# Kernel optimization log

Hardware: AMD Instinct MI355X
Metric: run time of the kernel (lower is better)

## Reference

```python
import jax, jax.numpy as jnp
import numpy as np

N = 256      # n_nodes (complete graph -> E = N*N edges)
HID = 128    # hid_dim
L = 4        # num_layers
NCAT = 64    # number of edge-orbit categories
CIN, COUT = 2, 3
B = 8
E = N * N


def _ln(x, g, b, eps=1e-5):
    m = x.mean(-1, keepdims=True)
    v = ((x - m) ** 2).mean(-1, keepdims=True)
    return (x - m) * jax.lax.rsqrt(v + eps) * g + b


def _mlp(x, W1, b1, g1, bt1, W2, b2, g2, bt2):
    # Linear -> LayerNorm -> ReLU -> Linear -> LayerNorm
    h = jax.nn.relu(_ln(x @ W1 + b1, g1, bt1))
    return _ln(h @ W2 + b2, g2, bt2)


def setup_inputs() -> dict:
    key = jax.random.key(0)
    ks = jax.random.split(key, 10)
    s = 0.05
    ii = jnp.arange(N, dtype=jnp.int32)
    edge_src = jnp.repeat(ii, N)   # i of (i,j), matches [(i,j) for i for j]
    edge_dst = jnp.tile(ii, N)     # j of (i,j)
    edge_cat = jax.random.randint(ks[0], (E,), 0, NCAT, dtype=jnp.int32)
    return dict(
        x=jax.random.normal(ks[1], (B, N, CIN), jnp.float32),
        emb=jax.random.normal(ks[2], (NCAT, HID), jnp.float32),
        in_W1=jax.random.normal(ks[3], (CIN, HID), jnp.float32) * s,
        in_b1=jnp.zeros(HID), in_g1=jnp.ones(HID), in_bt1=jnp.zeros(HID),
        in_W2=jax.random.normal(ks[4], (HID, HID), jnp.float32) * s,
        in_b2=jnp.zeros(HID), in_g2=jnp.ones(HID), in_bt2=jnp.zeros(HID),
        conv_W1=jax.random.normal(ks[5], (L, HID, HID), jnp.float32) * s,
        conv_b1=jnp.zeros((L, HID)), conv_g1=jnp.ones((L, HID)), conv_bt1=jnp.zeros((L, HID)),
        conv_W2=jax.random.normal(ks[6], (L, HID, HID), jnp.float32) * s,
        conv_b2=jnp.zeros((L, HID)), conv_g2=jnp.ones((L, HID)), conv_bt2=jnp.zeros((L, HID)),
        conv_eps=jnp.zeros(L),
        ln_g=jnp.ones((L, HID)), ln_b=jnp.zeros((L, HID)),
        out_W=jax.random.normal(ks[7], (HID, COUT), jnp.float32) * s,
        out_b=jnp.zeros(COUT),
        edge_src=edge_src, edge_dst=edge_dst, edge_cat=edge_cat,
    )


def reference(x, emb, in_W1, in_b1, in_g1, in_bt1, in_W2, in_b2, in_g2, in_bt2,
              conv_W1, conv_b1, conv_g1, conv_bt1, conv_W2, conv_b2, conv_g2, conv_bt2,
              conv_eps, ln_g, ln_b, out_W, out_b, edge_src, edge_dst, edge_cat):
    # EdgeEmbedder: per-category max-norm clip (all norms = 1.0 in the dense path)
    e = emb[edge_cat]                                  # [E, HID]
    cn = jnp.linalg.norm(e, axis=1, keepdims=True)
    cn = jnp.where(cn == 0, 1e-8, cn)
    e = e * jnp.minimum(1.0, 1.0 / cn)

    def item(xi):                                      # xi: [N, CIN]
        h = _mlp(xi, in_W1, in_b1, in_g1, in_bt1, in_W2, in_b2, in_g2, in_bt2)
        for l in range(L):
            # GINEConv: msg = relu(x_j + e_ij), aggregate (sum) at destination
            msg = jax.nn.relu(h[edge_src] + e)          # [E, HID]
            agg = jax.ops.segment_sum(msg, edge_dst, num_segments=N)
            h2 = _mlp((1.0 + conv_eps[l]) * h + agg,
                      conv_W1[l], conv_b1[l], conv_g1[l], conv_bt1[l],
                      conv_W2[l], conv_b2[l], conv_g2[l], conv_bt2[l])
            h = jax.nn.relu(_ln(h2, ln_g[l], ln_b[l])) + h
        return h @ out_W + out_b                        # [N, COUT]

    return jax.vmap(item)(x)                            # [B, N, COUT]
```

## Files before the change

### kernel.cpp

```cpp
#include <hip/hip_runtime.h>

#define HID 128
#define NN  256
#define BB  8
#define NCATS 64

__device__ inline void ln_stats(float a, float c, float& mean, float& rs) {
    float s = a + c;
    float q = a * a + c * c;
    #pragma unroll
    for (int m = 32; m; m >>= 1) {
        s += __shfl_xor(s, m);
        q += __shfl_xor(q, m);
    }
    mean = s * (1.0f / 128.0f);
    float var = q * (1.0f / 128.0f) - mean * mean;
    rs = rsqrtf(var + 1e-5f);
}

__global__ __launch_bounds__(512) void k_setup(
    const float* __restrict__ x, const float* __restrict__ emb,
    const float* __restrict__ inW1, const float* __restrict__ inb1,
    const float* __restrict__ ing1, const float* __restrict__ inbt1,
    const float* __restrict__ inW2, const float* __restrict__ inb2,
    const float* __restrict__ ing2, const float* __restrict__ inbt2,
    const int* __restrict__ ecat,
    float* __restrict__ ne, uint2* __restrict__ catp, float* __restrict__ h0)
{
    __shared__ __align__(16) float sV[8][128];
    __shared__ __align__(16) float sH1[8][128];
    __shared__ __align__(16) float sA[4][8][128];

    const int blk = blockIdx.x;
    const int t = threadIdx.x;
    const int w = t >> 6, lane = t & 63;

    if (blk < 256) {
        const int row0 = blk * 8;
        for (int item = t; item < 1024; item += 512) {
            int r = item >> 7, dd = item & 127;
            int row = row0 + r;
            float x0 = x[row * 2 + 0], x1 = x[row * 2 + 1];
            sV[r][dd] = fmaf(x0, inW1[dd], fmaf(x1, inW1[128 + dd], inb1[dd]));
        }
        __syncthreads();
        {
            float a = sV[w][lane], c = sV[w][lane + 64];
            float mean, rs; ln_stats(a, c, mean, rs);
            sH1[w][lane]      = fmaxf((a - mean) * rs * ing1[lane]      + inbt1[lane],      0.f);
            sH1[w][lane + 64] = fmaxf((c - mean) * rs * ing1[lane + 64] + inbt1[lane + 64], 0.f);
        }
        __syncthreads();
        {
            int dd = t & 127, ks = t >> 7;
            float acc[8] = {0.f, 0.f, 0.f, 0.f, 0.f, 0.f, 0.f, 0.f};
            for (int k = ks * 32; k < ks * 32 + 32; ++k) {
                float wv = inW2[k * 128 + dd];
                #pragma unroll
                for (int r = 0; r < 8; ++r) acc[r] = fmaf(sH1[r][k], wv, acc[r]);
            }
            #pragma unroll
            for (int r = 0; r < 8; ++r) sA[ks][r][dd] = acc[r];
        }
        __syncthreads();
        for (int item = t; item < 1024; item += 512) {
            int r = item >> 7, dd = item & 127;
            sV[r][dd] = inb2[dd] + sA[0][r][dd] + sA[1][r][dd] + sA[2][r][dd] + sA[3][r][dd];
        }
        __syncthreads();
        {
            float a = sV[w][lane], c = sV[w][lane + 64];
            float mean, rs; ln_stats(a, c, mean, rs);
            int row = row0 + w;
            h0[row * HID + lane]      = (a - mean) * rs * ing2[lane]      + inbt2[lane];
            h0[row * HID + lane + 64] = (c - mean) * rs * ing2[lane + 64] + inbt2[lane + 64];
        }
    } else if (blk < 264) {
        int r = (blk - 256) * 8 + w;
        float a = emb[r * 128 + lane], c = emb[r * 128 + lane + 64];
        float q = a * a + c * c;
        #pragma unroll
        for (int m = 32; m; m >>= 1) q += __shfl_xor(q, m);
        float cn = sqrtf(q);
        if (cn == 0.f) cn = 1e-8f;
        float sc = fminf(1.0f, 1.0f / cn);
        ne[r * 128 + lane]      = a * sc;
        ne[r * 128 + lane + 64] = c * sc;
    } else {
        int jb = blk - 264;
        if (t < 256) {
            int i = t;
            const int* p = ecat + i * NN + jb * 8;
            int4 c0 = *(const int4*)p;
            int4 c1 = *(const int4*)(p + 4);
            unsigned lo = (unsigned)c0.x | ((unsigned)c0.y << 8) |
                          ((unsigned)c0.z << 16) | ((unsigned)c0.w << 24);
            unsigned hi = (unsigned)c1.x | ((unsigned)c1.y << 8) |
                          ((unsigned)c1.z << 16) | ((unsigned)c1.w << 24);
            catp[jb * 256 + i] = make_uint2(lo, hi);
        }
    }
}

__global__ __launch_bounds__(512) void k_layer(
    const float* __restrict__ h_old, float* __restrict__ h_new,
    const float* __restrict__ ne, const uint2* __restrict__ catp,
    const float* __restrict__ W1, const float* __restrict__ b1,
    const float* __restrict__ g1, const float* __restrict__ bt1,
    const float* __restrict__ W2, const float* __restrict__ b2,
    const float* __restrict__ g2, const float* __restrict__ bt2,
    const float* __restrict__ epsp,
    const float* __restrict__ lng, const float* __restrict__ lnb,
    const float* __restrict__ outW, const float* __restrict__ outb,
    float* __restrict__ dout, int isLast)
{
    __shared__ __align__(16) float sNe[NCATS * HID];
    __shared__ __align__(16) float sAcc[16 * 8 * 128];
    __shared__ __align__(16) uint2 sCat[256];
    __shared__ __align__(16) float sU[8][128];
    __shared__ __align__(16) float sH1[8][128];
    __shared__ __align__(16) float sV[8][128];

    const int t = threadIdx.x;
    const int b = blockIdx.x >> 5;
    const int jb = blockIdx.x & 31;
    const int w = t >> 6, lane = t & 63;
    const float* hb = h_old + (size_t)b * NN * HID;

    for (int idx = t; idx < NCATS * HID / 4; idx += 512)
        ((float4*)sNe)[idx] = ((const float4*)ne)[idx];
    if (t < 256) sCat[t] = catp[jb * 256 + t];
    __syncthreads();

    const int dg = t & 31;
    const int ig = t >> 5;
    float4 acc[8];
    #pragma unroll
    for (int k = 0; k < 8; ++k) acc[k] = make_float4(0.f, 0.f, 0.f, 0.f);

    for (int n = 0; n < 16; ++n) {
        int i = ig * 16 + n;
        float4 hv = *(const float4*)(hb + i * HID + dg * 4);
        uint2 c8 = sCat[i];
        #pragma unroll
        for (int k = 0; k < 8; ++k) {
            unsigned c = ((k < 4 ? (c8.x >> (8 * k)) : (c8.y >> (8 * (k - 4)))) & 255u);
            float4 nv = *(const float4*)&sNe[c * HID + dg * 4];
            acc[k].x += fmaxf(hv.x + nv.x, 0.f);
            acc[k].y += fmaxf(hv.y + nv.y, 0.f);
            acc[k].z += fmaxf(hv.z + nv.z, 0.f);
            acc[k].w += fmaxf(hv.w + nv.w, 0.f);
        }
    }
    #pragma unroll
    for (int k = 0; k < 8; ++k)
        *(float4*)&sAcc[(ig * 8 + k) * 128 + dg * 4] = acc[k];
    __syncthreads();

    const float eps1 = 1.0f + epsp[0];
    for (int item = t; item < 1024; item += 512) {
        int r = item >> 7, dd = item & 127;
        float s = 0.f;
        #pragma unroll
        for (int igx = 0; igx < 16; ++igx) s += sAcc[(igx * 8 + r) * 128 + dd];
        sU[r][dd] = eps1 * hb[(jb * 8 + r) * HID + dd] + s;
    }
    __syncthreads();

    {
        int dd = t & 127, ks = t >> 7;
        float a8[8] = {0.f, 0.f, 0.f, 0.f, 0.f, 0.f, 0.f, 0.f};
        for (int k = ks * 32; k < ks * 32 + 32; ++k) {
            float wv = W1[k * 128 + dd];
            #pragma unroll
            for (int r = 0; r < 8; ++r) a8[r] = fmaf(sU[r][k], wv, a8[r]);
        }
        #pragma unroll
        for (int r = 0; r < 8; ++r) sAcc[(ks * 8 + r) * 128 + dd] = a8[r];
    }
    __syncthreads();
    for (int item = t; item < 1024; item += 512) {
        int r = item >> 7, dd = item & 127;
        sV[r][dd] = b1[dd] + sAcc[r * 128 + dd] + sAcc[(8 + r) * 128 + dd] +
                    sAcc[(16 + r) * 128 + dd] + sAcc[(24 + r) * 128 + dd];
    }
    __syncthreads();

    {
        float a = sV[w][lane], c = sV[w][lane + 64];
        float mean, rs; ln_stats(a, c, mean, rs);
        sH1[w][lane]      = fmaxf((a - mean) * rs * g1[lane]      + bt1[lane],      0.f);
        sH1[w][lane + 64] = fmaxf((c - mean) * rs * g1[lane + 64] + bt1[lane + 64], 0.f);
    }
    __syncthreads();

    {
        int dd = t & 127, ks = t >> 7;
        float a8[8] = {0.f, 0.f, 0.f, 0.f, 0.f, 0.f, 0.f, 0.f};
        for (int k = ks * 32; k < ks * 32 + 32; ++k) {
            float wv = W2[k * 128 + dd];
            #pragma unroll
            for (int r = 0; r < 8; ++r) a8[r] = fmaf(sH1[r][k], wv, a8[r]);
        }
        #pragma unroll
        for (int r = 0; r < 8; ++r) sAcc[(ks * 8 + r) * 128 + dd] = a8[r];
    }
    __syncthreads();
    for (int item = t; item < 1024; item += 512) {
        int r = item >> 7, dd = item & 127;
        sV[r][dd] = b2[dd] + sAcc[r * 128 + dd] + sAcc[(8 + r) * 128 + dd] +
                    sAcc[(16 + r) * 128 + dd] + sAcc[(24 + r) * 128 + dd];
    }
    __syncthreads();

    {
        float a = sV[w][lane], c = sV[w][lane + 64];
        float mean, rs; ln_stats(a, c, mean, rs);
        float y1 = (a - mean) * rs * g2[lane]      + bt2[lane];
        float y2 = (c - mean) * rs * g2[lane + 64] + bt2[lane + 64];

        float mean3, rs3; ln_stats(y1, y2, mean3, rs3);
        int row = jb * 8 + w;
        int grow = b * NN + row;
        float ho1 = hb[row * HID + lane], ho2 = hb[row * HID + lane + 64];
        float z1 = fmaxf((y1 - mean3) * rs3 * lng[lane]      + lnb[lane],      0.f) + ho1;
        float z2 = fmaxf((y2 - mean3) * rs3 * lng[lane + 64] + lnb[lane + 64], 0.f) + ho2;

        if (!isLast) {
            h_new[(size_t)grow * HID + lane]      = z1;
            h_new[(size_t)grow * HID + lane + 64] = z2;
        } else {
            #pragma unroll
            for (int cc = 0; cc < 3; ++cc) {
                float p = z1 * outW[lane * 3 + cc] + z2 * outW[(lane + 64) * 3 + cc];
                #pragma unroll
                for (int m = 32; m; m >>= 1) p += __shfl_xor(p, m);
                if (lane == 0) dout[grow * 3 + cc] = p + outb[cc];
            }
        }
    }
}

extern "C" void kernel_launch(void* const* d_in, const int* in_sizes, int n_in,
                              void* d_out, int out_size, void* d_ws, size_t ws_size,
                              hipStream_t stream) {
    const float* x     = (const float*)d_in[0];
    const float* emb   = (const float*)d_in[1];
    const float* inW1  = (const float*)d_in[2];
    const float* inb1  = (const float*)d_in[3];
    const float* ing1  = (const float*)d_in[4];
    const float* inbt1 = (const float*)d_in[5];
    const float* inW2  = (const float*)d_in[6];
    const float* inb2  = (const float*)d_in[7];
    const float* ing2  = (const float*)d_in[8];
    const float* inbt2 = (const float*)d_in[9];
    const float* cW1   = (const float*)d_in[10];
    const float* cb1   = (const float*)d_in[11];
    const float* cg1   = (const float*)d_in[12];
    const float* cbt1  = (const float*)d_in[13];
    const float* cW2   = (const float*)d_in[14];
    const float* cb2   = (const float*)d_in[15];
    const float* cg2   = (const float*)d_in[16];
    const float* cbt2  = (const float*)d_in[17];
    const float* ceps  = (const float*)d_in[18];
    const float* lng   = (const float*)d_in[19];
    const float* lnb   = (const float*)d_in[20];
    const float* outW  = (const float*)d_in[21];
    const float* outb  = (const float*)d_in[22];
    const int*   ecat  = (const int*)d_in[25];

    float* ws   = (float*)d_ws;
    float* ne   = ws;
    uint2* catp = (uint2*)(ws + 8192);
    float* hA   = ws + 8192 + 16384;
    float* hB   = hA + BB * NN * HID;
    float* out  = (float*)d_out;

    k_setup<<<296, 512, 0, stream>>>(x, emb, inW1, inb1, ing1, inbt1,
                                     inW2, inb2, ing2, inbt2, ecat, ne, catp, hA);

    for (int l = 0; l < 4; ++l) {
        const float* ho = (l & 1) ? hB : hA;
        float*       hn = (l & 1) ? hA : hB;
        k_layer<<<256, 512, 0, stream>>>(
            ho, hn, ne, catp,
            cW1 + l * HID * HID, cb1 + l * HID, cg1 + l * HID, cbt1 + l * HID,
            cW2 + l * HID * HID, cb2 + l * HID, cg2 + l * HID, cbt2 + l * HID,
            ceps + l, lng + l * HID, lnb + l * HID,
            outW, outb, out, (l == 3) ? 1 : 0);
    }
}
```

Before: 74.44 us.

## Fuse setup and all layers into one cooperative kernel with bf16 operands

Merges the setup kernel and the four layer kernels into one persistent cooperative kernel that uses grid.sync between layers. It also stores the normalized edge embeddings and the matmul activations as bf16 in shared memory, and pads the embedding layout. The gather partial sums are now reduced with a cross-half shuffle, which halves the shared-memory partial buffer. This removes launch overhead and the global round-trip for the embedding and category tables, at the cost of bf16 precision loss and a dependence on cooperative-launch support, with a multi-launch fallback.

```diff
diff --git a/kernel.cpp b/kernel.cpp
--- a/kernel.cpp
+++ b/kernel.cpp
@@ -1,9 +1,22 @@
 #include <hip/hip_runtime.h>
+#include <hip/hip_cooperative_groups.h>
+
+namespace cg = cooperative_groups;
 
 #define HID 128
 #define NN  256
 #define BB  8
 #define NCATS 64
+
+__device__ inline unsigned pack_bf16(float lo, float hi) {
+    unsigned ul = __float_as_uint(lo);
+    unsigned uh = __float_as_uint(hi);
+    ul = (ul + 0x7fffu + ((ul >> 16) & 1u)) >> 16;
+    uh = (uh + 0x7fffu + ((uh >> 16) & 1u)) & 0xffff0000u;
+    return ul | uh;
+}
+__device__ inline float bf_lo(unsigned v) { return __uint_as_float(v << 16); }
+__device__ inline float bf_hi(unsigned v) { return __uint_as_float(v & 0xffff0000u); }
 
 __device__ inline void ln_stats(float a, float c, float& mean, float& rs) {
     float s = a + c;
@@ -18,275 +31,333 @@
     rs = rsqrtf(var + 1e-5f);
 }
 
-__global__ __launch_bounds__(512) void k_setup(
-    const float* __restrict__ x, const float* __restrict__ emb,
-    const float* __restrict__ inW1, const float* __restrict__ inb1,
-    const float* __restrict__ ing1, const float* __restrict__ inbt1,
-    const float* __restrict__ inW2, const float* __restrict__ inb2,
-    const float* __restrict__ ing2, const float* __restrict__ inbt2,
-    const int* __restrict__ ecat,
-    float* __restrict__ ne, uint2* __restrict__ catp, float* __restrict__ h0)
+struct KArgs {
+    const float* x; const float* emb;
+    const float* inW1; const float* inb1; const float* ing1; const float* inbt1;
+    const float* inW2; const float* inb2; const float* ing2; const float* inbt2;
+    const float* cW1; const float* cb1; const float* cg1; const float* cbt1;
+    const float* cW2; const float* cb2; const float* cg2; const float* cbt2;
+    const float* ceps; const float* lng; const float* lnb;
+    const float* outW; const float* outb;
+    const int* ecat;
+    float* hA; float* hB; float* dout;
+};
+
+__global__ __launch_bounds__(512, 2) void k_fused(KArgs a, int lbeg, int lend, int dosync)
 {
-    __shared__ __align__(16) float sV[8][128];
-    __shared__ __align__(16) float sH1[8][128];
-    __shared__ __align__(16) float sA[4][8][128];
-
-    const int blk = blockIdx.x;
-    const int t = threadIdx.x;
-    const int w = t >> 6, lane = t & 63;
-
-    if (blk < 256) {
-        const int row0 = blk * 8;
-        for (int item = t; item < 1024; item += 512) {
-            int r = item >> 7, dd = item & 127;
-            int row = row0 + r;
-            float x0 = x[row * 2 + 0], x1 = x[row * 2 + 1];
-            sV[r][dd] = fmaf(x0, inW1[dd], fmaf(x1, inW1[128 + dd], inb1[dd]));
-        }
-        __syncthreads();
-        {
-            float a = sV[w][lane], c = sV[w][lane + 64];
-            float mean, rs; ln_stats(a, c, mean, rs);
-            sH1[w][lane]      = fmaxf((a - mean) * rs * ing1[lane]      + inbt1[lane],      0.f);
-            sH1[w][lane + 64] = fmaxf((c - mean) * rs * ing1[lane + 64] + inbt1[lane + 64], 0.f);
-        }
-        __syncthreads();
-        {
-            int dd = t & 127, ks = t >> 7;
-            float acc[8] = {0.f, 0.f, 0.f, 0.f, 0.f, 0.f, 0.f, 0.f};
-            for (int k = ks * 32; k < ks * 32 + 32; ++k) {
-                float wv = inW2[k * 128 + dd];
-                #pragma unroll
-                for (int r = 0; r < 8; ++r) acc[r] = fmaf(sH1[r][k], wv, acc[r]);
-            }
-            #pragma unroll
-            for (int r = 0; r < 8; ++r) sA[ks][r][dd] = acc[r];
-        }
-        __syncthreads();
-        for (int item = t; item < 1024; item += 512) {
-            int r = item >> 7, dd = item & 127;
-            sV[r][dd] = inb2[dd] + sA[0][r][dd] + sA[1][r][dd] + sA[2][r][dd] + sA[3][r][dd];
-        }
-        __syncthreads();
-        {
-            float a = sV[w][lane], c = sV[w][lane + 64];
-            float mean, rs; ln_stats(a, c, mean, rs);
-            int row = row0 + w;
-            h0[row * HID + lane]      = (a - mean) * rs * ing2[lane]      + inbt2[lane];
-            h0[row * HID + lane + 64] = (c - mean) * rs * ing2[lane + 64] + inbt2[lane + 64];
-        }
-    } else if (blk < 264) {
-        int r = (blk - 256) * 8 + w;
-        float a = emb[r * 128 + lane], c = emb[r * 128 + lane + 64];
-        float q = a * a + c * c;
+    __shared__ __align__(16) uint4    sNe4[NCATS * 17];
+    __shared__ __align__(16) float    sPart[8 * 8 * 128];
+    __shared__ __align__(16) uint2    sCat[256];
+    __shared__ __align__(16) uint4    sUT[128];
+    __shared__ __align__(16) float    sH1[8][128];
+    __shared__ __align__(16) uint4    sH1T[128];
+    __shared__ __align__(16) float    sV[8][128];
+
+    cg::grid_group grid = cg::this_grid();
+
+    const int t  = threadIdx.x;
+    const int b  = blockIdx.x >> 5;
+    const int jg = blockIdx.x & 31;
+    const int w  = t >> 6, lane = t & 63;
+    const uint2* sNe2 = (const uint2*)sNe4;
+
+    #pragma unroll 1
+    for (int rr = 0; rr < 8; ++rr) {
+        int r = w * 8 + rr;
+        float2 em = *(const float2*)(a.emb + r * 128 + 2 * lane);
+        float q = em.x * em.x + em.y * em.y;
         #pragma unroll
         for (int m = 32; m; m >>= 1) q += __shfl_xor(q, m);
         float cn = sqrtf(q);
         if (cn == 0.f) cn = 1e-8f;
         float sc = fminf(1.0f, 1.0f / cn);
-        ne[r * 128 + lane]      = a * sc;
-        ne[r * 128 + lane + 64] = c * sc;
-    } else {
-        int jb = blk - 264;
-        if (t < 256) {
-            int i = t;
-            const int* p = ecat + i * NN + jb * 8;
-            int4 c0 = *(const int4*)p;
-            int4 c1 = *(const int4*)(p + 4);
-            unsigned lo = (unsigned)c0.x | ((unsigned)c0.y << 8) |
-                          ((unsigned)c0.z << 16) | ((unsigned)c0.w << 24);
-            unsigned hi = (unsigned)c1.x | ((unsigned)c1.y << 8) |
-                          ((unsigned)c1.z << 16) | ((unsigned)c1.w << 24);
-            catp[jb * 256 + i] = make_uint2(lo, hi);
-        }
-    }
-}
-
-__global__ __launch_bounds__(512) void k_layer(
-    const float* __restrict__ h_old, float* __restrict__ h_new,
-    const float* __restrict__ ne, const uint2* __restrict__ catp,
-    const float* __restrict__ W1, const float* __restrict__ b1,
-    const float* __restrict__ g1, const float* __restrict__ bt1,
-    const float* __restrict__ W2, const float* __restrict__ b2,
-    const float* __restrict__ g2, const float* __restrict__ bt2,
-    const float* __restrict__ epsp,
-    const float* __restrict__ lng, const float* __restrict__ lnb,
-    const float* __restrict__ outW, const float* __restrict__ outb,
-    float* __restrict__ dout, int isLast)
-{
-    __shared__ __align__(16) float sNe[NCATS * HID];
-    __shared__ __align__(16) float sAcc[16 * 8 * 128];
-    __shared__ __align__(16) uint2 sCat[256];
-    __shared__ __align__(16) float sU[8][128];
-    __shared__ __align__(16) float sH1[8][128];
-    __shared__ __align__(16) float sV[8][128];
-
-    const int t = threadIdx.x;
-    const int b = blockIdx.x >> 5;
-    const int jb = blockIdx.x & 31;
-    const int w = t >> 6, lane = t & 63;
-    const float* hb = h_old + (size_t)b * NN * HID;
-
-    for (int idx = t; idx < NCATS * HID / 4; idx += 512)
-        ((float4*)sNe)[idx] = ((const float4*)ne)[idx];
-    if (t < 256) sCat[t] = catp[jb * 256 + t];
+        ((unsigned*)sNe4)[r * 68 + lane] = pack_bf16(em.x * sc, em.y * sc);
+    }
+    if (t < 256) {
+        const int* p = a.ecat + t * NN + jg * 8;
+        int4 c0 = *(const int4*)p;
+        int4 c1 = *(const int4*)(p + 4);
+        unsigned lo = (unsigned)c0.x | ((unsigned)c0.y << 8) |
+                      ((unsigned)c0.z << 16) | ((unsigned)c0.w << 24);
+        unsigned hi = (unsigned)c1.x | ((unsigned)c1.y << 8) |
+                      ((unsigned)c1.z << 16) | ((unsigned)c1.w << 24);
+        sCat[t] = make_uint2(lo, hi);
+    }
     __syncthreads();
 
-    const int dg = t & 31;
-    const int ig = t >> 5;
-    float4 acc[8];
-    #pragma unroll
-    for (int k = 0; k < 8; ++k) acc[k] = make_float4(0.f, 0.f, 0.f, 0.f);
-
-    for (int n = 0; n < 16; ++n) {
-        int i = ig * 16 + n;
-        float4 hv = *(const float4*)(hb + i * HID + dg * 4);
-        uint2 c8 = sCat[i];
+    if (lbeg < 0) {
+        for (int item = t; item < 1024; item += 512) {
+            int r = item >> 7, d = item & 127;
+            int row = b * NN + jg * 8 + r;
+            float x0 = a.x[row * 2 + 0], x1 = a.x[row * 2 + 1];
+            sV[r][d] = fmaf(x0, a.inW1[d], fmaf(x1, a.inW1[128 + d], a.inb1[d]));
+        }
+        __syncthreads();
+        {
+            float aa = sV[w][lane], cc = sV[w][lane + 64];
+            float mean, rs; ln_stats(aa, cc, mean, rs);
+            sH1[w][lane]      = fmaxf((aa - mean) * rs * a.ing1[lane]      + a.inbt1[lane],      0.f);
+            sH1[w][lane + 64] = fmaxf((cc - mean) * rs * a.ing1[lane + 64] + a.inbt1[lane + 64], 0.f);
+        }
+        __syncthreads();
+        {
+            int dim = t & 127, q = t >> 7;
+            ((unsigned*)sH1T)[dim * 4 + q] = pack_bf16(sH1[2 * q][dim], sH1[2 * q + 1][dim]);
+        }
+        __syncthreads();
+        {
+            const int dd = t & 127, ks = t >> 7;
+            float a8[8] = {0.f,0.f,0.f,0.f,0.f,0.f,0.f,0.f};
+            #pragma unroll 8
+            for (int k = 0; k < 32; ++k) {
+                int kk = ks * 32 + k;
+                uint4 ax = sH1T[kk];
+                float wv = a.inW2[kk * 128 + dd];
+                a8[0] = fmaf(bf_lo(ax.x), wv, a8[0]);
+                a8[1] = fmaf(bf_hi(ax.x), wv, a8[1]);
+                a8[2] = fmaf(bf_lo(ax.y), wv, a8[2]);
+                a8[3] = fmaf(bf_hi(ax.y), wv, a8[3]);
+                a8[4] = fmaf(bf_lo(ax.z), wv, a8[4]);
+                a8[5] = fmaf(bf_hi(ax.z), wv, a8[5]);
+                a8[6] = fmaf(bf_lo(ax.w), wv, a8[6]);
+                a8[7] = fmaf(bf_hi(ax.w), wv, a8[7]);
+            }
+            #pragma unroll
+            for (int r = 0; r < 8; ++r) sPart[(ks * 8 + r) * 128 + dd] = a8[r];
+        }
+        __syncthreads();
+        for (int item = t; item < 1024; item += 512) {
+            int r = item >> 7, d = item & 127;
+            sV[r][d] = a.inb2[d] + sPart[r * 128 + d] + sPart[(8 + r) * 128 + d] +
+                       sPart[(16 + r) * 128 + d] + sPart[(24 + r) * 128 + d];
+        }
+        __syncthreads();
+        {
+            float aa = sV[w][lane], cc = sV[w][lane + 64];
+            float mean, rs; ln_stats(aa, cc, mean, rs);
+            int grow = b * NN + jg * 8 + w;
+            a.hA[grow * HID + lane]      = (aa - mean) * rs * a.ing2[lane]      + a.inbt2[lane];
+            a.hA[grow * HID + lane + 64] = (cc - mean) * rs * a.ing2[lane + 64] + a.inbt2[lane + 64];
+        }
+        if (dosync) grid.sync();
+    }
+
+    #pragma unroll 1
+    for (int l = (lbeg < 0 ? 0 : lbeg); l < lend; ++l) {
+        const float* h_old = (l & 1) ? a.hB : a.hA;
+        float*       h_new = (l & 1) ? a.hA : a.hB;
+        const float* W1  = a.cW1 + l * HID * HID;
+        const float* W2  = a.cW2 + l * HID * HID;
+        const float* b1  = a.cb1 + l * HID;
+        const float* b2  = a.cb2 + l * HID;
+        const float* g1  = a.cg1 + l * HID;
+        const float* bt1 = a.cbt1 + l * HID;
+        const float* g2  = a.cg2 + l * HID;
+        const float* bt2 = a.cbt2 + l * HID;
+        const float* lg  = a.lng + l * HID;
+        const float* lb  = a.lnb + l * HID;
+        const float* hb  = h_old + (size_t)b * NN * HID;
+        const int isLast = (l == 3);
+
+        const int dg = t & 31;
+        const int ig = t >> 5;
+        float acc[8][4];
         #pragma unroll
-        for (int k = 0; k < 8; ++k) {
-            unsigned c = ((k < 4 ? (c8.x >> (8 * k)) : (c8.y >> (8 * (k - 4)))) & 255u);
-            float4 nv = *(const float4*)&sNe[c * HID + dg * 4];
-            acc[k].x += fmaxf(hv.x + nv.x, 0.f);
-            acc[k].y += fmaxf(hv.y + nv.y, 0.f);
-            acc[k].z += fmaxf(hv.z + nv.z, 0.f);
-            acc[k].w += fmaxf(hv.w + nv.w, 0.f);
-        }
-    }
-    #pragma unroll
-    for (int k = 0; k < 8; ++k)
-        *(float4*)&sAcc[(ig * 8 + k) * 128 + dg * 4] = acc[k];
-    __syncthreads();
-
-    const float eps1 = 1.0f + epsp[0];
-    for (int item = t; item < 1024; item += 512) {
-        int r = item >> 7, dd = item & 127;
-        float s = 0.f;
+        for (int k = 0; k < 8; ++k)
+            #pragma unroll
+            for (int d = 0; d < 4; ++d) acc[k][d] = 0.f;
+
+        #pragma unroll 4
+        for (int n = 0; n < 16; ++n) {
+            int i = ig * 16 + n;
+            float4 hv = *(const float4*)(hb + i * HID + dg * 4);
+            uint2 c8 = sCat[i];
+            #pragma unroll
+            for (int k = 0; k < 8; ++k) {
+                unsigned c = ((k < 4 ? (c8.x >> (8 * k)) : (c8.y >> (8 * (k - 4)))) & 255u);
+                uint2 nv = sNe2[c * 34 + dg];
+                acc[k][0] += fmaxf(hv.x + bf_lo(nv.x), 0.f);
+                acc[k][1] += fmaxf(hv.y + bf_hi(nv.x), 0.f);
+                acc[k][2] += fmaxf(hv.z + bf_lo(nv.y), 0.f);
+                acc[k][3] += fmaxf(hv.w + bf_hi(nv.y), 0.f);
+            }
+        }
         #pragma unroll
-        for (int igx = 0; igx < 16; ++igx) s += sAcc[(igx * 8 + r) * 128 + dd];
-        sU[r][dd] = eps1 * hb[(jb * 8 + r) * HID + dd] + s;
-    }
-    __syncthreads();
-
-    {
-        int dd = t & 127, ks = t >> 7;
-        float a8[8] = {0.f, 0.f, 0.f, 0.f, 0.f, 0.f, 0.f, 0.f};
-        for (int k = ks * 32; k < ks * 32 + 32; ++k) {
-            float wv = W1[k * 128 + dd];
-            #pragma unroll
-            for (int r = 0; r < 8; ++r) a8[r] = fmaf(sU[r][k], wv, a8[r]);
-        }
-        #pragma unroll
-        for (int r = 0; r < 8; ++r) sAcc[(ks * 8 + r) * 128 + dd] = a8[r];
-    }
-    __syncthreads();
-    for (int item = t; item < 1024; item += 512) {
-        int r = item >> 7, dd = item & 127;
-        sV[r][dd] = b1[dd] + sAcc[r * 128 + dd] + sAcc[(8 + r) * 128 + dd] +
-                    sAcc[(16 + r) * 128 + dd] + sAcc[(24 + r) * 128 + dd];
-    }
-    __syncthreads();
-
-    {
-        float a = sV[w][lane], c = sV[w][lane + 64];
-        float mean, rs; ln_stats(a, c, mean, rs);
-        sH1[w][lane]      = fmaxf((a - mean) * rs * g1[lane]      + bt1[lane],      0.f);
-        sH1[w][lane + 64] = fmaxf((c - mean) * rs * g1[lane + 64] + bt1[lane + 64], 0.f);
-    }
-    __syncthreads();
-
-    {
-        int dd = t & 127, ks = t >> 7;
-        float a8[8] = {0.f, 0.f, 0.f, 0.f, 0.f, 0.f, 0.f, 0.f};
-        for (int k = ks * 32; k < ks * 32 + 32; ++k) {
-            float wv = W2[k * 128 + dd];
-            #pragma unroll
-            for (int r = 0; r < 8; ++r) a8[r] = fmaf(sH1[r][k], wv, a8[r]);
-        }
-        #pragma unroll
-        for (int r = 0; r < 8; ++r) sAcc[(ks * 8 + r) * 128 + dd] = a8[r];
-    }
-    __syncthreads();
-    for (int item = t; item < 1024; item += 512) {
-        int r = item >> 7, dd = item & 127;
-        sV[r][dd] = b2[dd] + sAcc[r * 128 + dd] + sAcc[(8 + r) * 128 + dd] +
-                    sAcc[(16 + r) * 128 + dd] + sAcc[(24 + r) * 128 + dd];
-    }
-    __syncthreads();
-
-    {
-        float a = sV[w][lane], c = sV[w][lane + 64];
-        float mean, rs; ln_stats(a, c, mean, rs);
-        float y1 = (a - mean) * rs * g2[lane]      + bt2[lane];
-        float y2 = (c - mean) * rs * g2[lane + 64] + bt2[lane + 64];
-
-        float mean3, rs3; ln_stats(y1, y2, mean3, rs3);
-        int row = jb * 8 + w;
-        int grow = b * NN + row;
-        float ho1 = hb[row * HID + lane], ho2 = hb[row * HID + lane + 64];
-        float z1 = fmaxf((y1 - mean3) * rs3 * lng[lane]      + lnb[lane],      0.f) + ho1;
-        float z2 = fmaxf((y2 - mean3) * rs3 * lng[lane + 64] + lnb[lane + 64], 0.f) + ho2;
-
-        if (!isLast) {
-            h_new[(size_t)grow * HID + lane]      = z1;
-            h_new[(size_t)grow * HID + lane + 64] = z2;
-        } else {
-            #pragma unroll
-            for (int cc = 0; cc < 3; ++cc) {
-                float p = z1 * outW[lane * 3 + cc] + z2 * outW[(lane + 64) * 3 + cc];
+        for (int k = 0; k < 8; ++k)
+            #pragma unroll
+            for (int d = 0; d < 4; ++d)
+                acc[k][d] += __shfl_xor(acc[k][d], 32);
+        {
+            int kb = ((t >> 5) & 1) * 4;
+            #pragma unroll
+            for (int k2 = 0; k2 < 4; ++k2)
+                *(float4*)&sPart[(w * 8 + kb + k2) * 128 + dg * 4] =
+                    make_float4(acc[kb + k2][0], acc[kb + k2][1],
+                                acc[kb + k2][2], acc[kb + k2][3]);
+        }
+        __syncthreads();
+
+        {
+            int dim = t & 127, q = t >> 7;
+            const float eps1 = 1.0f + a.ceps[l];
+            int r0 = 2 * q, r1 = 2 * q + 1;
+            float u0 = eps1 * hb[(jg * 8 + r0) * HID + dim];
+            float u1 = eps1 * hb[(jg * 8 + r1) * HID + dim];
+            #pragma unroll
+            for (int pg = 0; pg < 8; ++pg) {
+                u0 += sPart[(pg * 8 + r0) * 128 + dim];
+                u1 += sPart[(pg * 8 + r1) * 128 + dim];
+            }
+            ((unsigned*)sUT)[dim * 4 + q] = pack_bf16(u0, u1);
+        }
+        __syncthreads();
+
+        {
+            const int dd = t & 127, ks = t >> 7;
+            float a8[8] = {0.f,0.f,0.f,0.f,0.f,0.f,0.f,0.f};
+            #pragma unroll 8
+            for (int k = 0; k < 32; ++k) {
+                int kk = ks * 32 + k;
+                uint4 ax = sUT[kk];
+                float wv = W1[kk * 128 + dd];
+                a8[0] = fmaf(bf_lo(ax.x), wv, a8[0]);
+                a8[1] = fmaf(bf_hi(ax.x), wv, a8[1]);
+                a8[2] = fmaf(bf_lo(ax.y), wv, a8[2]);
+                a8[3] = fmaf(bf_hi(ax.y), wv, a8[3]);
+                a8[4] = fmaf(bf_lo(ax.z), wv, a8[4]);
+                a8[5] = fmaf(bf_hi(ax.z), wv, a8[5]);
+                a8[6] = fmaf(bf_lo(ax.w), wv, a8[6]);
+                a8[7] = fmaf(bf_hi(ax.w), wv, a8[7]);
+            }
+            #pragma unroll
+            for (int r = 0; r < 8; ++r) sPart[(ks * 8 + r) * 128 + dd] = a8[r];
+        }
+        __syncthreads();
+        for (int item = t; item < 1024; item += 512) {
+            int r = item >> 7, d = item & 127;
+            sV[r][d] = b1[d] + sPart[r * 128 + d] + sPart[(8 + r) * 128 + d] +
+                       sPart[(16 + r) * 128 + d] + sPart[(24 + r) * 128 + d];
+        }
+        __syncthreads();
+
+        {
+            float aa = sV[w][lane], cc = sV[w][lane + 64];
+            float mean, rs; ln_stats(aa, cc, mean, rs);
+            sH1[w][lane]      = fmaxf((aa - mean) * rs * g1[lane]      + bt1[lane],      0.f);
+            sH1[w][lane + 64] = fmaxf((cc - mean) * rs * g1[lane + 64] + bt1[lane + 64], 0.f);
+        }
+        __syncthreads();
+        {
+            int dim = t & 127, q = t >> 7;
+            ((unsigned*)sH1T)[dim * 4 + q] = pack_bf16(sH1[2 * q][dim], sH1[2 * q + 1][dim]);
+        }
+        __syncthreads();
+
+        {
+            const int dd = t & 127, ks = t >> 7;
+            float a8[8] = {0.f,0.f,0.f,0.f,0.f,0.f,0.f,0.f};
+            #pragma unroll 8
+            for (int k = 0; k < 32; ++k) {
+                int kk = ks * 32 + k;
+                uint4 ax = sH1T[kk];
+                float wv = W2[kk * 128 + dd];
+                a8[0] = fmaf(bf_lo(ax.x), wv, a8[0]);
+                a8[1] = fmaf(bf_hi(ax.x), wv, a8[1]);
+                a8[2] = fmaf(bf_lo(ax.y), wv, a8[2]);
+                a8[3] = fmaf(bf_hi(ax.y), wv, a8[3]);
+                a8[4] = fmaf(bf_lo(ax.z), wv, a8[4]);
+                a8[5] = fmaf(bf_hi(ax.z), wv, a8[5]);
+                a8[6] = fmaf(bf_lo(ax.w), wv, a8[6]);
+                a8[7] = fmaf(bf_hi(ax.w), wv, a8[7]);
+            }
+            #pragma unroll
+            for (int r = 0; r < 8; ++r) sPart[(ks * 8 + r) * 128 + dd] = a8[r];
+        }
+        __syncthreads();
+        for (int item = t; item < 1024; item += 512) {
+            int r = item >> 7, d = item & 127;
+            sV[r][d] = b2[d] + sPart[r * 128 + d] + sPart[(8 + r) * 128 + d] +
+                       sPart[(16 + r) * 128 + d] + sPart[(24 + r) * 128 + d];
+        }
+        __syncthreads();
+
+        {
+            float aa = sV[w][lane], cc = sV[w][lane + 64];
+            float mean, rs; ln_stats(aa, cc, mean, rs);
+            float y1 = (aa - mean) * rs * g2[lane]      + bt2[lane];
+            float y2 = (cc - mean) * rs * g2[lane + 64] + bt2[lane + 64];
+
+            float mean3, rs3; ln_stats(y1, y2, mean3, rs3);
+            int row = jg * 8 + w;
+            int grow = b * NN + row;
+            float ho1 = hb[row * HID + lane], ho2 = hb[row * HID + lane + 64];
+            float z1 = fmaxf((y1 - mean3) * rs3 * lg[lane]      + lb[lane],      0.f) + ho1;
+            float z2 = fmaxf((y2 - mean3) * rs3 * lg[lane + 64] + lb[lane + 64], 0.f) + ho2;
+
+            if (!isLast) {
+                h_new[(size_t)grow * HID + lane]      = z1;
+                h_new[(size_t)grow * HID + lane + 64] = z2;
+            } else {
                 #pragma unroll
-                for (int m = 32; m; m >>= 1) p += __shfl_xor(p, m);
-                if (lane == 0) dout[grow * 3 + cc] = p + outb[cc];
-            }
-        }
+                for (int ccx = 0; ccx < 3; ++ccx) {
+                    float p = z1 * a.outW[lane * 3 + ccx] + z2 * a.outW[(lane + 64) * 3 + ccx];
+                    #pragma unroll
+                    for (int m = 32; m; m >>= 1) p += __shfl_xor(p, m);
+                    if (lane == 0) a.dout[grow * 3 + ccx] = p + a.outb[ccx];
+                }
+            }
+        }
+        if (dosync && l < 3) grid.sync();
     }
 }
 
 extern "C" void kernel_launch(void* const* d_in, const int* in_sizes, int n_in,
                               void* d_out, int out_size, void* d_ws, size_t ws_size,
                               hipStream_t stream) {
-    const float* x     = (const float*)d_in[0];
-    const float* emb   = (const float*)d_in[1];
-    const float* inW1  = (const float*)d_in[2];
-    const float* inb1  = (const float*)d_in[3];
-    const float* ing1  = (const float*)d_in[4];
-    const float* inbt1 = (const float*)d_in[5];
-    const float* inW2  = (const float*)d_in[6];
-    const float* inb2  = (const float*)d_in[7];
-    const float* ing2  = (const float*)d_in[8];
-    const float* inbt2 = (const float*)d_in[9];
-    const float* cW1   = (const float*)d_in[10];
-    const float* cb1   = (const float*)d_in[11];
-    const float* cg1   = (const float*)d_in[12];
-    const float* cbt1  = (const float*)d_in[13];
-    const float* cW2   = (const float*)d_in[14];
-    const float* cb2   = (const float*)d_in[15];
-    const float* cg2   = (const float*)d_in[16];
-    const float* cbt2  = (const float*)d_in[17];
-    const float* ceps  = (const float*)d_in[18];
-    const float* lng   = (const float*)d_in[19];
-    const float* lnb   = (const float*)d_in[20];
-    const float* outW  = (const float*)d_in[21];
-    const float* outb  = (const float*)d_in[22];
-    const int*   ecat  = (const int*)d_in[25];
-
-    float* ws   = (float*)d_ws;
-    float* ne   = ws;
-    uint2* catp = (uint2*)(ws + 8192);
-    float* hA   = ws + 8192 + 16384;
-    float* hB   = hA + BB * NN * HID;
-    float* out  = (float*)d_out;
-
-    k_setup<<<296, 512, 0, stream>>>(x, emb, inW1, inb1, ing1, inbt1,
-                                     inW2, inb2, ing2, inbt2, ecat, ne, catp, hA);
-
-    for (int l = 0; l < 4; ++l) {
-        const float* ho = (l & 1) ? hB : hA;
-        float*       hn = (l & 1) ? hA : hB;
-        k_layer<<<256, 512, 0, stream>>>(
-            ho, hn, ne, catp,
-            cW1 + l * HID * HID, cb1 + l * HID, cg1 + l * HID, cbt1 + l * HID,
-            cW2 + l * HID * HID, cb2 + l * HID, cg2 + l * HID, cbt2 + l * HID,
-            ceps + l, lng + l * HID, lnb + l * HID,
-            outW, outb, out, (l == 3) ? 1 : 0);
-    }
+    float* ws = (float*)d_ws;
+    KArgs ka;
+    ka.x     = (const float*)d_in[0];
+    ka.emb   = (const float*)d_in[1];
+    ka.inW1  = (const float*)d_in[2];
+    ka.inb1  = (const float*)d_in[3];
+    ka.ing1  = (const float*)d_in[4];
+    ka.inbt1 = (const float*)d_in[5];
+    ka.inW2  = (const float*)d_in[6];
+    ka.inb2  = (const float*)d_in[7];
+    ka.ing2  = (const float*)d_in[8];
+    ka.inbt2 = (const float*)d_in[9];
+    ka.cW1   = (const float*)d_in[10];
+    ka.cb1   = (const float*)d_in[11];
+    ka.cg1   = (const float*)d_in[12];
+    ka.cbt1  = (const float*)d_in[13];
+    ka.cW2   = (const float*)d_in[14];
+    ka.cb2   = (const float*)d_in[15];
+    ka.cg2   = (const float*)d_in[16];
+    ka.cbt2  = (const float*)d_in[17];
+    ka.ceps  = (const float*)d_in[18];
+    ka.lng   = (const float*)d_in[19];
+    ka.lnb   = (const float*)d_in[20];
+    ka.outW  = (const float*)d_in[21];
+    ka.outb  = (const float*)d_in[22];
+    ka.ecat  = (const int*)d_in[25];
+    ka.hA    = ws;
+    ka.hB    = ws + BB * NN * HID;
+    ka.dout  = (float*)d_out;
+
+    int nb = 0;
+    hipError_t oe = hipOccupancyMaxActiveBlocksPerMultiprocessor(&nb, k_fused, 512, 0);
+    bool coop_ok = (oe == hipSuccess && nb >= 1);
+
+    if (coop_ok) {
+        int lbeg = -1, lend = 4, dosync = 1;
+        void* kp[] = { (void*)&ka, (void*)&lbeg, (void*)&lend, (void*)&dosync };
+        hipError_t le = hipLaunchCooperativeKernel((const void*)k_fused,
+                                                   dim3(256), dim3(512), kp, 0, stream);
+        if (le == hipSuccess) return;
+    }
+    k_fused<<<256, 512, 0, stream>>>(ka, -1, 0, 0);
+    k_fused<<<256, 512, 0, stream>>>(ka, 0, 1, 0);
+    k_fused<<<256, 512, 0, stream>>>(ka, 1, 2, 0);
+    k_fused<<<256, 512, 0, stream>>>(ka, 2, 3, 0);
+    k_fused<<<256, 512, 0, stream>>>(ka, 3, 4, 0);
 }
```

After: 137.3 us. 84.4% more time.
